# Kernel optimization log

Measured on AMD Instinct MI355X. Metric: run time of the kernel, lower is better.

Reference implementation:

```python
import math
import jax, jax.numpy as jnp
import numpy as np
from jax import lax

B, S, T = 16, 1200, 600
D, V, FF = 1024, 1404, 2048
H, DH, PERIOD, WID = 4, 256, 25, 8


def setup_inputs() -> dict:
    key = jax.random.key(0)
    ks = jax.random.split(key, 24)
    w = lambda i, shape: jax.random.normal(ks[i], shape, dtype=jnp.float32) * 0.02
    return {
        "audio_embedding": jax.random.normal(ks[0], (B, S, 768), dtype=jnp.float32),
        "vertice": jax.random.normal(ks[1], (B, T, 3, 468), dtype=jnp.float32),
        "W_af": w(2, (D, 768)), "b_af": w(3, (D,)),
        "sa_Wq": w(4, (D, D)), "sa_bq": w(5, (D,)),
        "sa_Wk": w(6, (D, D)), "sa_bk": w(7, (D,)),
        "sa_Wv": w(8, (D, D)), "sa_bv": w(9, (D,)),
        "sa_Wo": w(10, (D, D)), "sa_bo": w(11, (D,)),
        "ca_Wq": w(12, (D, D)), "ca_bq": w(13, (D,)),
        "ca_Wk": w(14, (D, D)), "ca_bk": w(15, (D,)),
        "ca_Wv": w(16, (D, D)), "ca_bv": w(17, (D,)),
        "ca_Wo": w(18, (D, D)), "ca_bo": w(19, (D,)),
        "ln1_g": jnp.ones((D,), jnp.float32), "ln1_b": jnp.zeros((D,), jnp.float32),
        "ln2_g": jnp.ones((D,), jnp.float32), "ln2_b": jnp.zeros((D,), jnp.float32),
        "ln3_g": jnp.ones((D,), jnp.float32), "ln3_b": jnp.zeros((D,), jnp.float32),
        "W_ff1": w(20, (FF, D)), "b_ff1": jnp.zeros((FF,), jnp.float32),
        "W_ff2": w(21, (D, FF)), "b_ff2": jnp.zeros((D,), jnp.float32),
        "W_vm": w(22, (D, V)), "b_vm": jnp.zeros((D,), jnp.float32),
        "W_vr": w(23, (V, D)), "b_vr": jnp.zeros((V,), jnp.float32),
    }


def _pe_table():
    # PeriodicPositionalEncoding: sin/cos table of length `period`, tiled over time
    pos = np.arange(PERIOD, dtype=np.float32)[:, None]
    div = np.exp(np.arange(0, D, 2, dtype=np.float32) * (-math.log(10000.0) / D))
    pe = np.zeros((PERIOD, D), dtype=np.float32)
    pe[:, 0::2] = np.sin(pos * div)
    pe[:, 1::2] = np.cos(pos * div)
    return jnp.asarray(pe)


def _slopes():
    start = 2.0 ** (-2.0 ** (-(math.log2(H) - 3.0)))
    return jnp.asarray(start * start ** np.arange(H, dtype=np.float32), dtype=jnp.float32)


def _ln(x, g, b):
    m = jnp.mean(x, -1, keepdims=True)
    v = jnp.mean((x - m) ** 2, -1, keepdims=True)
    return (x - m) / jnp.sqrt(v + 1e-5) * g + b


def reference(audio_embedding, vertice, W_af, b_af, sa_Wq, sa_bq, sa_Wk, sa_bk, sa_Wv, sa_bv, sa_Wo, sa_bo, ca_Wq, ca_bq, ca_Wk, ca_bk, ca_Wv, ca_bv, ca_Wo, ca_bo, ln1_g, ln1_b, ln2_g, ln2_b, ln3_g, ln3_b, W_ff1, b_ff1, W_ff2, b_ff2, W_vm, b_vm, W_vr, b_vr):
    # The torch loop reruns the full causal decoder on the growing prefix each frame;
    # because the tgt mask is strictly causal (ALiBi bias depends only on i-j), the
    # math is exactly equivalent to an incremental decode with a self-attn KV cache.
    pe, slopes = _pe_table(), _slopes()
    scale = 1.0 / math.sqrt(DH)
    NEG = -1e9
    hidden = audio_embedding @ W_af.T + b_af              # (B,S,D) audio_feature_map
    mem_k = (hidden @ ca_Wk.T + ca_bk).reshape(B, S, H, DH)
    mem_v = (hidden @ ca_Wv.T + ca_bv).reshape(B, S, H, DH)
    t_idx = jnp.arange(T)
    s_idx = jnp.arange(S)
    emb0 = jnp.broadcast_to(b_vm, (B, D))                 # vertice_map(zeros)
    kc0 = jnp.zeros((T, B, D), jnp.float32)
    vc0 = jnp.zeros((T, B, D), jnp.float32)

    def step(carry, i):
        emb, kc, vc = carry
        x = emb + pe[i % PERIOD]                          # PPE (B,D)
        q = (x @ sa_Wq.T + sa_bq).reshape(B, H, DH)
        kc = kc.at[i].set(x @ sa_Wk.T + sa_bk)
        vc = vc.at[i].set(x @ sa_Wv.T + sa_bv)
        kh = kc.reshape(T, B, H, DH)
        vh = vc.reshape(T, B, H, DH)
        rel = i - t_idx                                   # ALiBi: alibi[i,j] = -floor((i-j)/period)
        bias = slopes[:, None] * (-(jnp.maximum(rel, 0) // PERIOD)).astype(jnp.float32)
        sc = jnp.einsum('bhd,tbhd->bht', q, kh) * scale + bias[None]
        sc = jnp.where((t_idx <= i)[None, None, :], sc, NEG)
        sa = jnp.einsum('bht,tbhd->bhd', jax.nn.softmax(sc, -1), vh).reshape(B, D)
        x = _ln(x + sa @ sa_Wo.T + sa_bo, ln1_g, ln1_b)
        q2 = (x @ ca_Wq.T + ca_bq).reshape(B, H, DH)
        sc2 = jnp.einsum('bhd,bshd->bhs', q2, mem_k) * scale
        allowed = (s_idx >= 2 * i - (WID - 2)) & (s_idx < 2 * i + 2)   # enc_dec_mask window
        sc2 = jnp.where(allowed[None, None, :], sc2, NEG)
        ca = jnp.einsum('bhs,bshd->bhd', jax.nn.softmax(sc2, -1), mem_v).reshape(B, D)
        x = _ln(x + ca @ ca_Wo.T + ca_bo, ln2_g, ln2_b)
        ff = jax.nn.relu(x @ W_ff1.T + b_ff1) @ W_ff2.T + b_ff2
        x = _ln(x + ff, ln3_g, ln3_b)
        out_v = x @ W_vr.T + b_vr                         # vertice_map_r (B,V)
        emb_next = out_v @ W_vm.T + b_vm                  # vertice_map of last output
        return (emb_next, kc, vc), out_v

    _, outs = lax.scan(step, (emb0, kc0, vc0), t_idx)
    vertice_out = jnp.transpose(outs, (1, 0, 2))          # (B,T,V)
    loss = jnp.mean((vertice_out - vertice.reshape(B, T, -1)) ** 2)
    return loss
```

## Files before the change

### kernel.cpp

```cpp
#include <hip/hip_runtime.h>

typedef unsigned short u16;
typedef short s16x8 __attribute__((ext_vector_type(8)));
typedef float f32x4 __attribute__((ext_vector_type(4)));
typedef float f32x2 __attribute__((ext_vector_type(2)));

#define DEV static __device__ __forceinline__

DEV float bf2f(u16 h){ union{unsigned u;float f;} v; v.u=((unsigned)h)<<16; return v.f; }
DEV u16 f2bf(float f){ union{float f;unsigned u;} v; v.f=f; unsigned u=v.u; return (u16)((u + 0x7fffu + ((u>>16)&1u))>>16); }

DEV void st2_dc(u16* p, u16 v){
  unsigned vv = v;
  asm volatile("global_store_short %0, %1, off sc0 sc1" :: "v"(p), "v"(vv) : "memory");
}
DEV void st16_dc(void* p, s16x8 v){
  asm volatile("global_store_dwordx4 %0, %1, off sc0 sc1" :: "v"(p), "v"(v) : "memory");
}
DEV void stf_dc(float* p, float v){
  asm volatile("global_store_dword %0, %1, off sc0 sc1" :: "v"(p), "v"(v) : "memory");
}
DEV u16 ld2_dc(const u16* p){
  unsigned r;
  asm volatile("global_load_ushort %0, %1, off sc0 sc1\n\ts_waitcnt vmcnt(0)" : "=&v"(r) : "v"(p) : "memory");
  return (u16)r;
}
DEV void vmwait0(){ asm volatile("s_waitcnt vmcnt(0)" ::: "memory"); }

DEV void ldf8_dc(const u16* p, s16x8* o){
  asm volatile(
    "global_load_dwordx4 %0, %8, off sc0 sc1\n\t"
    "global_load_dwordx4 %1, %8, off offset:64 sc0 sc1\n\t"
    "global_load_dwordx4 %2, %8, off offset:128 sc0 sc1\n\t"
    "global_load_dwordx4 %3, %8, off offset:192 sc0 sc1\n\t"
    "global_load_dwordx4 %4, %8, off offset:256 sc0 sc1\n\t"
    "global_load_dwordx4 %5, %8, off offset:320 sc0 sc1\n\t"
    "global_load_dwordx4 %6, %8, off offset:384 sc0 sc1\n\t"
    "global_load_dwordx4 %7, %8, off offset:448 sc0 sc1\n\t"
    "s_waitcnt vmcnt(0)"
    : "=&v"(o[0]),"=&v"(o[1]),"=&v"(o[2]),"=&v"(o[3]),
      "=&v"(o[4]),"=&v"(o[5]),"=&v"(o[6]),"=&v"(o[7])
    : "v"(p) : "memory");
}
DEV void ldf8r_dc(const u16* p, s16x8* o, const u16* pr, unsigned* rr){
  asm volatile(
    "global_load_dwordx4 %0, %9, off sc0 sc1\n\t"
    "global_load_dwordx4 %1, %9, off offset:64 sc0 sc1\n\t"
    "global_load_dwordx4 %2, %9, off offset:128 sc0 sc1\n\t"
    "global_load_dwordx4 %3, %9, off offset:192 sc0 sc1\n\t"
    "global_load_dwordx4 %4, %9, off offset:256 sc0 sc1\n\t"
    "global_load_dwordx4 %5, %9, off offset:320 sc0 sc1\n\t"
    "global_load_dwordx4 %6, %9, off offset:384 sc0 sc1\n\t"
    "global_load_dwordx4 %7, %9, off offset:448 sc0 sc1\n\t"
    "global_load_ushort %8, %10, off sc0 sc1\n\t"
    "s_waitcnt vmcnt(0)"
    : "=&v"(o[0]),"=&v"(o[1]),"=&v"(o[2]),"=&v"(o[3]),
      "=&v"(o[4]),"=&v"(o[5]),"=&v"(o[6]),"=&v"(o[7]),"=&v"(*rr)
    : "v"(p), "v"(pr) : "memory");
}
DEV void ldf8rs_dc(const u16* p, s16x8* o, const u16* pr, unsigned* rr, const float* ps, f32x2* ss){
  asm volatile(
    "global_load_dwordx4 %0, %10, off sc0 sc1\n\t"
    "global_load_dwordx4 %1, %10, off offset:64 sc0 sc1\n\t"
    "global_load_dwordx4 %2, %10, off offset:128 sc0 sc1\n\t"
    "global_load_dwordx4 %3, %10, off offset:192 sc0 sc1\n\t"
    "global_load_dwordx4 %4, %10, off offset:256 sc0 sc1\n\t"
    "global_load_dwordx4 %5, %10, off offset:320 sc0 sc1\n\t"
    "global_load_dwordx4 %6, %10, off offset:384 sc0 sc1\n\t"
    "global_load_dwordx4 %7, %10, off offset:448 sc0 sc1\n\t"
    "global_load_ushort %8, %11, off sc0 sc1\n\t"
    "global_load_dwordx2 %9, %12, off sc0 sc1\n\t"
    "s_waitcnt vmcnt(0)"
    : "=&v"(o[0]),"=&v"(o[1]),"=&v"(o[2]),"=&v"(o[3]),
      "=&v"(o[4]),"=&v"(o[5]),"=&v"(o[6]),"=&v"(o[7]),"=&v"(*rr),"=&v"(*ss)
    : "v"(p), "v"(pr), "v"(ps) : "memory");
}
DEV void ldf16rs_dc(const u16* p, s16x8* o, const u16* pr, unsigned* rr, const float* ps, f32x2* ss){
  asm volatile(
    "global_load_dwordx4 %0, %18, off sc0 sc1\n\t"
    "global_load_dwordx4 %1, %18, off offset:64 sc0 sc1\n\t"
    "global_load_dwordx4 %2, %18, off offset:128 sc0 sc1\n\t"
    "global_load_dwordx4 %3, %18, off offset:192 sc0 sc1\n\t"
    "global_load_dwordx4 %4, %18, off offset:256 sc0 sc1\n\t"
    "global_load_dwordx4 %5, %18, off offset:320 sc0 sc1\n\t"
    "global_load_dwordx4 %6, %18, off offset:384 sc0 sc1\n\t"
    "global_load_dwordx4 %7, %18, off offset:448 sc0 sc1\n\t"
    "global_load_dwordx4 %8, %18, off offset:2048 sc0 sc1\n\t"
    "global_load_dwordx4 %9, %18, off offset:2112 sc0 sc1\n\t"
    "global_load_dwordx4 %10, %18, off offset:2176 sc0 sc1\n\t"
    "global_load_dwordx4 %11, %18, off offset:2240 sc0 sc1\n\t"
    "global_load_dwordx4 %12, %18, off offset:2304 sc0 sc1\n\t"
    "global_load_dwordx4 %13, %18, off offset:2368 sc0 sc1\n\t"
    "global_load_dwordx4 %14, %18, off offset:2432 sc0 sc1\n\t"
    "global_load_dwordx4 %15, %18, off offset:2496 sc0 sc1\n\t"
    "global_load_ushort %16, %19, off sc0 sc1\n\t"
    "global_load_dwordx2 %17, %20, off sc0 sc1\n\t"
    "s_waitcnt vmcnt(0)"
    : "=&v"(o[0]),"=&v"(o[1]),"=&v"(o[2]),"=&v"(o[3]),
      "=&v"(o[4]),"=&v"(o[5]),"=&v"(o[6]),"=&v"(o[7]),
      "=&v"(o[8]),"=&v"(o[9]),"=&v"(o[10]),"=&v"(o[11]),
      "=&v"(o[12]),"=&v"(o[13]),"=&v"(o[14]),"=&v"(o[15]),
      "=&v"(*rr),"=&v"(*ss)
    : "v"(p), "v"(pr), "v"(ps) : "memory");
}

constexpr size_t SZ_DD = (size_t)1024*1024*2;
constexpr size_t OFF_WQ=0;
constexpr size_t OFF_WK=OFF_WQ+SZ_DD;
constexpr size_t OFF_WV=OFF_WK+SZ_DD;
constexpr size_t OFF_WO=OFF_WV+SZ_DD;
constexpr size_t OFF_CAWQ=OFF_WO+SZ_DD;
constexpr size_t OFF_CAWO=OFF_CAWQ+SZ_DD;
constexpr size_t OFF_FF1=OFF_CAWO+SZ_DD;
constexpr size_t OFF_FF2=OFF_FF1+(size_t)2048*1024*2;
constexpr size_t OFF_MB =OFF_FF2+(size_t)2048*1024*2;
constexpr size_t OFF_WVR=OFF_MB+SZ_DD;
constexpr size_t OFF_WKP=OFF_WVR+(size_t)1404*1024*2;
constexpr size_t OFF_WVP=OFF_WKP+(size_t)1024*768*2;
constexpr size_t OFF_WAFT=OFF_WVP+(size_t)1024*768*2;
constexpr size_t OFF_WVRT=OFF_WAFT+(size_t)768*1024*2;
constexpr size_t OFF_PE  =OFF_WVRT+(size_t)1024*1408*2;
constexpr size_t OFF_BKP =OFF_PE+25*1024*4;
constexpr size_t OFF_BVP =OFF_BKP+4096;
constexpr size_t OFF_BCOMB=OFF_BVP+4096;
constexpr size_t OFF_MEMK=OFF_BCOMB+4096;
constexpr size_t OFF_MEMV=OFF_MEMK+(size_t)16*1200*1024*2;
constexpr size_t OFF_KC  =OFF_MEMV+(size_t)16*1200*1024*2;
constexpr size_t OFF_VC  =OFF_KC+(size_t)600*16*1024*2;
constexpr size_t OFF_U3S =OFF_VC+(size_t)600*16*1024*2;
constexpr size_t OFF_ST3 =OFF_U3S+(size_t)600*16*1024*2;
constexpr size_t OFF_EMB =OFF_ST3+600*32*4;
constexpr size_t OFF_QB  =OFF_EMB+32768;
constexpr size_t OFF_SC  =OFF_QB+32768;
constexpr size_t OFF_SA  =OFF_SC+(size_t)16*4*608*4;
constexpr size_t OFF_U1  =OFF_SA+32768;
constexpr size_t OFF_ST1 =OFF_U1+32768;
constexpr size_t OFF_Q2  =OFF_ST1+256;
constexpr size_t OFF_CA  =OFF_Q2+32768;
constexpr size_t OFF_U2  =OFF_CA+32768;
constexpr size_t OFF_ST2 =OFF_U2+32768;
constexpr size_t OFF_HH  =OFF_ST2+256;
constexpr size_t OFF_LOSS=OFF_HH+65536;
constexpr size_t OFF_BAR =OFF_LOSS+256;
constexpr size_t WS_NEED =OFF_BAR+32768;

DEV float gemm_frag(const s16x8* a, const u16* slot, float* FB){
  int tid=threadIdx.x, wv=tid>>6, ln=tid&63;
  int r=ln&15, kq=ln>>4;
  int k0=wv*256 + kq*8;
  int sw=(r&7)<<3;
  const u16* bp = slot + r*1024;
  f32x4 acc={0.f,0.f,0.f,0.f};
  #pragma unroll
  for(int j=0;j<8;j++)
    acc = __builtin_amdgcn_mfma_f32_16x16x32_bf16(a[j], *(const s16x8*)(bp + ((k0+32*j)^sw)), acc, 0,0,0);
  #pragma unroll
  for(int j=0;j<4;j++) FB[wv*256 + (kq*4+j)*16 + r] = acc[j];
  __syncthreads();
  int row=tid>>4, col=tid&15;
  float s=(FB[row*16+col]+FB[256+row*16+col])+(FB[512+row*16+col]+FB[768+row*16+col]);
  __syncthreads();
  return s;
}

DEV void ln_frags(s16x8* a, const float* g, const float* be, int k0, int r, float* RB, float* STm, float* STr){
  int tid=threadIdx.x;
  float sum=0.f, sq=0.f;
  #pragma unroll
  for(int j=0;j<8;j++){
    #pragma unroll
    for(int e=0;e<8;e++){ float f=bf2f((u16)a[j][e]); sum+=f; sq+=f*f; }
  }
  RB[tid]=sum; RB[256+tid]=sq;
  __syncthreads();
  if (tid<16){
    float S=0.f,Q=0.f;
    #pragma unroll
    for(int q=0;q<16;q++){ S+=RB[tid+16*q]; Q+=RB[256+tid+16*q]; }
    float m=S*(1.f/1024.f); float var=Q*(1.f/1024.f)-m*m;
    STm[tid]=m; STr[tid]=rsqrtf(var+1e-5f);
  }
  __syncthreads();
  float m=STm[r], rs=STr[r];
  const float* gg=g+k0; const float* bb=be+k0;
  #pragma unroll
  for(int j=0;j<8;j++){
    s16x8 o;
    #pragma unroll
    for(int e=0;e<8;e++){ int k=32*j+e; float f=(bf2f((u16)a[j][e])-m)*rs*gg[k]+bb[k]; o[e]=(short)f2bf(f); }
    a[j]=o;
  }
}

DEV void copy_slot(const u16* src, int rstride, u16* dst){
  int row=threadIdx.x>>4, k0=(threadIdx.x&15)<<6;
  int sw=(row&7)<<3;
  const u16* s = src + (size_t)row*rstride + k0;
  u16* d = dst + row*1024;
  #pragma unroll
  for(int c=0;c<64;c+=8)
    *(s16x8*)(d + (((k0+c))^sw)) = *(const s16x8*)(s+c);
}

DEV void gbar(char* barb, unsigned& epoch, int wg){
  vmwait0();
  __syncthreads();
  unsigned target = epoch + 1u;
  if (threadIdx.x == 0)
    __hip_atomic_store((unsigned*)(barb + (wg<<7)), target, __ATOMIC_RELAXED, __HIP_MEMORY_SCOPE_AGENT);
  {
    unsigned* s = (unsigned*)(barb + (threadIdx.x<<7));
    while (__hip_atomic_load(s, __ATOMIC_RELAXED, __HIP_MEMORY_SCOPE_AGENT) < target)
      __builtin_amdgcn_s_sleep(1);
  }
  __syncthreads();
  epoch++;
}

__global__ void __launch_bounds__(256) k_init(const float* b_vm, float* pe, u16* emb, float* loss, unsigned* bar){
  int tid=threadIdx.x;
  if (tid==0) loss[0]=0.f;
  for(int idx=tid; idx<8192; idx+=256) bar[idx]=0u;
  for(int idx=tid; idx<16384; idx+=256) emb[idx] = f2bf(b_vm[idx&1023]);
  for(int idx=tid; idx<25600; idx+=256){
    int p_=idx>>10, d_=idx&1023; int m=d_>>1;
    float div = expf(-(float)(2*m) * (9.210340372f/1024.f));
    float a = (float)p_ * div;
    pe[idx] = (d_&1)? cosf(a) : sinf(a);
  }
}

__global__ void __launch_bounds__(256) k_f2bf(const float* s, u16* d, int n){
  int idx=(blockIdx.x*256+threadIdx.x)*8;
  if (idx < n){
    #pragma unroll
    for(int j=0;j<8;j++) d[idx+j]=f2bf(s[idx+j]);
  }
}

__global__ void __launch_bounds__(256) k_tr(const float* src, int R, int C, u16* dst, int ldd){
  __shared__ float TL[32][33];
  int cb=(C+31)/32;
  int bj=blockIdx.x%cb, br=blockIdx.x/cb;
  int j0=bj*32, r0=br*32;
  int lj=threadIdx.x&31, lr=threadIdx.x>>5;
  #pragma unroll
  for(int p=0;p<4;p++){ int rr=r0+lr+p*8, jj=j0+lj;
    TL[lr+p*8][lj] = (rr<R && jj<C)? src[(size_t)rr*C+jj] : 0.f; }
  __syncthreads();
  #pragma unroll
  for(int p=0;p<4;p++){ int jj=j0+lr+p*8, rr=r0+lj;
    if (jj<C && rr<ldd) dst[(size_t)jj*ldd+rr] = f2bf(TL[lj][lr+p*8]); }
}

DEV float gemm_tile16g(const u16* SLu, int lds_stride, const u16* W, int Kext, int wstride, int colbase, float* FB){
  int tid=threadIdx.x, wv=tid>>6, ln=tid&63;
  int r=ln&15, kq=ln>>4;
  int kpw=Kext>>2, k0=wv*kpw;
  const u16* ap = SLu + r*lds_stride + k0 + kq*8;
  const u16* bp = W + (size_t)(colbase+r)*wstride + k0 + kq*8;
  f32x4 acc={0.f,0.f,0.f,0.f};
  for(int k=0;k<kpw;k+=32)
    acc = __builtin_amdgcn_mfma_f32_16x16x32_bf16(*(const s16x8*)(ap+k), *(const s16x8*)(bp+k), acc, 0,0,0);
  #pragma unroll
  for(int j=0;j<4;j++) FB[wv*256 + (kq*4+j)*16 + r] = acc[j];
  __syncthreads();
  int row=tid>>4, col=tid&15;
  float s=(FB[row*16+col]+FB[256+row*16+col])+(FB[512+row*16+col]+FB[768+row*16+col]);
  __syncthreads();
  return s;
}

__global__ void __launch_bounds__(256) k_gemm_pre(const float* A, int lda, int Kreal, int Kpad,
                                                  const u16* Bw, u16* out, int ldo, int Ntiles){
  __shared__ u16 SL[16*1416];
  __shared__ float FB[1024];
  int bx=blockIdx.x; int mt=bx/Ntiles, nt=bx%Ntiles;
  int tid=threadIdx.x;
  int cpt = Kpad>>4;
  { int row=tid>>4, c0=(tid&15)*cpt;
    const float* s=A + (size_t)(mt*16+row)*lda;
    u16* d=SL + row*(Kpad+8);
    for(int c=0;c<cpt;c++){ int k=c0+c; d[k] = (k<Kreal)? f2bf(s[k]) : (u16)0; }
    __syncthreads();
  }
  float v = gemm_tile16g(SL, Kpad+8, Bw, Kpad, Kpad, nt*16, FB);
  int row=tid>>4, col=tid&15;
  out[(size_t)(mt*16+row)*ldo + nt*16+col] = f2bf(v);
}

__global__ void __launch_bounds__(256) k_bvec(const float* caWk, const float* ca_bk, const float* b_af,
                                              const float* caWv, const float* ca_bv,
                                              const float* Wvm, const float* b_vr, const float* b_vm,
                                              float* bkp, float* bvp, float* bcomb){
  __shared__ float VB[1408];
  int seg=blockIdx.x>>2, ch=blockIdx.x&3; int o=ch*256+threadIdx.x;
  const float* vec = (seg==2)? b_vr : b_af; int K = (seg==2)?1404:1024;
  for(int k=threadIdx.x;k<K;k+=256) VB[k]=vec[k];
  __syncthreads();
  const float* Arow = (seg==0)? caWk+(size_t)o*1024 : (seg==1)? caWv+(size_t)o*1024 : Wvm+(size_t)o*1404;
  float s=0.f;
  for(int k=0;k<K;k++) s += Arow[k]*VB[k];
  if(seg==0) bkp[o]=s+ca_bk[o]; else if(seg==1) bvp[o]=s+ca_bv[o]; else bcomb[o]=s+b_vm[o];
}

__global__ void __launch_bounds__(256) k_mem(const float* audio, const u16* wkp, const u16* wvp,
                                             const float* bkp, const float* bvp, u16* mt8, u16* memv){
  __shared__ u16 SL[16*776];
  int bx=blockIdx.x; int mt=bx>>3, cbk=bx&7;
  int tid=threadIdx.x, wv=tid>>6, ln=tid&63;
  { int row=tid>>4, c0=(tid&15)*48;
    const float* s = audio + (size_t)(mt*16+row)*768 + c0;
    u16* d = SL + row*776 + c0;
    #pragma unroll
    for(int c=0;c<48;c+=8){ s16x8 o;
      #pragma unroll
      for(int j=0;j<8;j++) o[j]=(short)f2bf(s[c+j]);
      *(s16x8*)(d+c)=o; }
    __syncthreads();
  }
  int r=ln&15, kq=ln>>4;
  const u16* ap = SL + r*776 + kq*8;
  for(int rep=0;rep<2;rep++){
    int colb = cbk*128 + wv*32 + rep*16;
    for(int mat=0;mat<2;mat++){
      const u16* W = mat? wvp : wkp;
      const u16* bp = W + (size_t)(colb+r)*768 + kq*8;
      f32x4 acc={0.f,0.f,0.f,0.f};
      for(int k=0;k<768;k+=32)
        acc = __builtin_amdgcn_mfma_f32_16x16x32_bf16(*(const s16x8*)(ap+k), *(const s16x8*)(bp+k), acc, 0,0,0);
      const float* bias = mat? bvp:bkp;
      int o = colb + r;
      float bo = bias[o];
      #pragma unroll
      for(int j=0;j<4;j++){ int row_=kq*4+j;
        int g = mt*16+row_;
        float val = acc[j] + bo;
        if (mat){
          memv[(size_t)g*1024 + o] = f2bf(val);
        } else {
          int bb=g/1200, ss=g-bb*1200;
          mt8[(((size_t)(bb*4 + (o>>8))*32 + ((o&255)>>3))*1200 + ss)*8 + (o&7)] = f2bf(val);
        }
      }
    }
  }
}

struct LoopArgs {
  const float *sa_bq,*sa_bk,*sa_bv,*sa_bo,*ca_bq,*ca_bo,*b_ff1,*b_ff2;
  const float *g1,*be1,*g2,*be2,*g3,*be3;
  char* ws;
};

__global__ void __launch_bounds__(256,1) k_loop(LoopArgs A){
  __shared__ u16 WL[3*16*1024];
  __shared__ float FB[1024];
  __shared__ float PL[608];
  __shared__ float RB[640];
  __shared__ float STm[16], STr[16];

  char* ws = A.ws;
  const u16* wq   =(const u16*)(ws+OFF_WQ);
  const u16* wk   =(const u16*)(ws+OFF_WK);
  const u16* wv_  =(const u16*)(ws+OFF_WV);
  const u16* wo   =(const u16*)(ws+OFF_WO);
  const u16* cawq =(const u16*)(ws+OFF_CAWQ);
  const u16* cawo =(const u16*)(ws+OFF_CAWO);
  const u16* ff1  =(const u16*)(ws+OFF_FF1);
  const u16* ff2  =(const u16*)(ws+OFF_FF2);
  const u16* mb   =(const u16*)(ws+OFF_MB);
  const float* pe =(const float*)(ws+OFF_PE);
  const float* bcomb=(const float*)(ws+OFF_BCOMB);
  const u16* mt8  =(const u16*)(ws+OFF_MEMK);
  const u16* memv =(const u16*)(ws+OFF_MEMV);
  u16* kc =(u16*)(ws+OFF_KC);
  u16* vc =(u16*)(ws+OFF_VC);
  u16* u3s=(u16*)(ws+OFF_U3S);
  float* st3=(float*)(ws+OFF_ST3);
  u16* emb=(u16*)(ws+OFF_EMB);
  u16* qb =(u16*)(ws+OFF_QB);
  u16* sab=(u16*)(ws+OFF_SA);
  u16* u1 =(u16*)(ws+OFF_U1);
  float* st1=(float*)(ws+OFF_ST1);
  u16* q2b=(u16*)(ws+OFF_Q2);
  u16* cab=(u16*)(ws+OFF_CA);
  u16* u2 =(u16*)(ws+OFF_U2);
  float* st2=(float*)(ws+OFF_ST2);
  u16* hh =(u16*)(ws+OFF_HH);
  char* barb=(char*)(ws+OFF_BAR);

  unsigned epoch = 0;
  int wg = blockIdx.x, tid = threadIdx.x;
  int row = tid>>4, lo = tid&15;
  int wv = tid>>6, ln = tid&63;
  int fr = ln&15, kq = ln>>4;
  int k0 = wv*256 + kq*8;
  int grp = wg>>6, ct = (wg&63)<<4;

  {
    u16* s0d = WL;          u16* s1d = WL+16384;  u16* s2d = WL+32768;
    if (grp==0){
      copy_slot(wq  +(size_t)ct*1024,1024,s0d);
      copy_slot(cawq+(size_t)ct*1024,1024,s1d);
      copy_slot(ff1 +(size_t)ct*1024,1024,s2d);
    } else if (grp==1){
      copy_slot(wk  +(size_t)ct*1024,1024,s0d);
      copy_slot(cawo+(size_t)ct*1024,1024,s1d);
      copy_slot(ff1 +((size_t)(1024+ct))*1024,1024,s2d);
    } else if (grp==2){
      copy_slot(wv_ +(size_t)ct*1024,1024,s0d);
      copy_slot(ff2 +(size_t)ct*2048,2048,s1d);
      copy_slot(ff2 +(size_t)ct*2048+1024,2048,s2d);
    } else {
      copy_slot(wo  +(size_t)ct*1024,1024,s0d);
      copy_slot(mb  +(size_t)ct*1024,1024,s1d);
    }
    __syncthreads();
  }
  const u16* SLOT0 = WL;
  const u16* SLOT1 = WL+16384;
  const u16* SLOT2 = WL+32768;

  #pragma unroll 1
  for (int i=0;i<600;i++){
    int ip = i%25;

    if (wg < 192){
      s16x8 f[8];
      ldf8_dc(emb + fr*1024 + k0, f);
      const float* pp = pe + ip*1024 + k0;
      #pragma unroll
      for(int j=0;j<8;j++){ s16x8 o;
        #pragma unroll
        for(int e=0;e<8;e++) o[e]=(short)f2bf(bf2f((u16)f[j][e]) + pp[32*j+e]);
        f[j]=o; }
      const float* bias = (grp==0)? A.sa_bq : (grp==1)? A.sa_bk : A.sa_bv;
      float v = gemm_frag(f,SLOT0,FB);
      int o = ct + lo;
      u16 bv = f2bf(v + bias[o]);
      if (grp==0)      st2_dc(qb + row*1024 + o, bv);
      else if (grp==1) st2_dc(kc + ((size_t)i*16+row)*1024 + o, bv);
      else             st2_dc(vc + ((size_t)i*16+row)*1024 + o, bv);
    }
    gbar(barb, epoch, wg);

    if (wg < 64){
      int b=wg>>2, h=wg&3, cnt=i+1;
      RB[tid] = bf2f(ld2_dc(qb + b*1024 + h*256 + tid));
      __syncthreads();
      float sl = 1.0f/(float)(4<<(2*h));
      float mloc=-1e30f, lloc=0.f;
      for(int t=tid; t<cnt; t+=256){
        const u16* kr = kc + ((size_t)t*16 + b)*1024 + h*256;
        float s=0.f;
        #pragma unroll
        for(int c=0;c<256;c+=8){
          s16x8 k8 = *(const s16x8*)(kr+c);
          #pragma unroll
          for(int j=0;j<8;j++) s += RB[c+j]*bf2f((u16)k8[j]);
        }
        s = s*0.0625f - sl*(float)((i-t)/25);
        PL[t]=s;
        float M = fmaxf(mloc, s);
        lloc = lloc*__expf(mloc-M) + __expf(s-M);
        mloc = M;
      }
      #pragma unroll
      for(int off=32; off>0; off>>=1){
        float m2=__shfl_xor(mloc,off), l2=__shfl_xor(lloc,off);
        float M=fmaxf(mloc,m2);
        lloc = lloc*__expf(mloc-M) + l2*__expf(m2-M);
        mloc = M;
      }
      if (ln==0){ RB[576+2*wv]=mloc; RB[577+2*wv]=lloc; }
      __syncthreads();
      float M=-1e30f, L=0.f;
      #pragma unroll
      for(int w=0;w<4;w++){
        float m2=RB[576+2*w], l2=RB[577+2*w];
        float Mn=fmaxf(M,m2);
        L = L*__expf(M-Mn) + l2*__expf(m2-Mn);
        M = Mn;
      }
      float rl = 1.0f/L;
      int d_oct = tid>>3, t_ln = tid&7;
      const u16* vcb = vc + (size_t)b*1024 + h*256 + d_oct*8;
      float acc[8]={0.f,0.f,0.f,0.f,0.f,0.f,0.f,0.f};
      for(int t=t_ln; t<cnt; t+=8){
        s16x8 v8 = *(const s16x8*)(vcb + (size_t)t*16384);
        float p = __expf(PL[t]-M);
        #pragma unroll
        for(int jj=0;jj<8;jj++) acc[jj] += p*bf2f((u16)v8[jj]);
      }
      #pragma unroll
      for(int j=0;j<8;j++){
        acc[j] += __shfl_xor(acc[j],1);
        acc[j] += __shfl_xor(acc[j],2);
        acc[j] += __shfl_xor(acc[j],4);
      }
      if (t_ln==0){
        s16x8 o8;
        #pragma unroll
        for(int j=0;j<8;j++) o8[j]=(short)f2bf(acc[j]*rl);
        st16_dc(sab + b*1024 + h*256 + d_oct*8, o8);
      }
    }
    gbar(barb, epoch, wg);

    if (wg>=192){
      s16x8 f[8]; unsigned er;
      ldf8r_dc(sab + fr*1024 + k0, f, emb + row*1024 + ct + lo, &er);
      float v = gemm_frag(f,SLOT0,FB);
      int o = ct+lo;
      float x = bf2f((u16)er) + pe[ip*1024+o];
      st2_dc(u1 + row*1024 + o, f2bf(x + v + A.sa_bo[o]));
    }
    gbar(barb, epoch, wg);

    if (wg<64){
      s16x8 f[8];
      ldf8_dc(u1 + fr*1024 + k0, f);
      ln_frags(f, A.g1, A.be1, k0, fr, RB, STm, STr);
      float v = gemm_frag(f,SLOT1,FB);
      int o=ct+lo;
      st2_dc(q2b + row*1024+o, f2bf(v + A.ca_bq[o]));
      if (wg==0 && tid<16){ stf_dc(st1+tid*2, STm[tid]); stf_dc(st1+tid*2+1, STr[tid]); }
    }
    gbar(barb, epoch, wg);

    if (wg<64){
      int b=wg>>2, h=wg&3;
      RB[tid] = bf2f(ld2_dc(q2b + b*1024 + h*256 + tid));
      __syncthreads();
      int s0 = 2*i-6; if(s0<0)s0=0;
      int s1 = 2*i+2; if(s1>1200)s1=1200;
      int ns = s1-s0;
      int si=tid>>5, dl=tid&31;
      float p=0.f;
      if (si<ns){
        const u16* MT = mt8 + (((size_t)(b*4+h)*32 + dl)*1200 + (s0+si))*8;
        s16x8 m8 = *(const s16x8*)MT;
        #pragma unroll
        for(int j=0;j<8;j++) p += RB[dl*8+j]*bf2f((u16)m8[j]);
      }
      #pragma unroll
      for(int o2=16;o2>0;o2>>=1) p += __shfl_xor(p,o2);
      if (dl==0 && si<ns) RB[512+si] = p*0.0625f;
      __syncthreads();
      float mx=-1e30f;
      for(int q=0;q<ns;q++) mx=fmaxf(mx,RB[512+q]);
      float l=0.f, acc=0.f;
      for(int q=0;q<ns;q++){
        float e=__expf(RB[512+q]-mx); l+=e;
        acc += e*bf2f(memv[(size_t)(b*1200+s0+q)*1024 + h*256 + tid]);
      }
      st2_dc(cab + b*1024+h*256+tid, f2bf(acc/l));
    }
    gbar(barb, epoch, wg);

    if (wg>=64 && wg<128){
      s16x8 f[8]; unsigned ur; f32x2 sv;
      ldf8rs_dc(cab + fr*1024 + k0, f, u1 + row*1024 + ct + lo, &ur, st1 + row*2, &sv);
      float v = gemm_frag(f,SLOT1,FB);
      int o=ct+lo;
      float x1 = (bf2f((u16)ur)-sv[0])*sv[1]*A.g1[o] + A.be1[o];
      st2_dc(u2+row*1024+o, f2bf(x1 + v + A.ca_bo[o]));
    }
    gbar(barb, epoch, wg);

    if (wg<128){
      s16x8 f[8];
      ldf8_dc(u2 + fr*1024 + k0, f);
      ln_frags(f, A.g2, A.be2, k0, fr, RB, STm, STr);
      float v = gemm_frag(f,SLOT2,FB);
      int o=(wg<<4)+lo;
      st2_dc(hh+row*2048+o, f2bf(fmaxf(v + A.b_ff1[o], 0.f)));
      if (wg==0 && tid<16){ stf_dc(st2+tid*2,STm[tid]); stf_dc(st2+tid*2+1,STr[tid]); }
    }
    gbar(barb, epoch, wg);

    if (wg>=128 && wg<192){
      s16x8 f[16]; unsigned ur; f32x2 sv;
      ldf16rs_dc(hh + fr*2048 + k0, f, u2 + row*1024 + ct + lo, &ur, st2 + row*2, &sv);
      float v = gemm_frag(f,SLOT1,FB);
      v += gemm_frag(f+8,SLOT2,FB);
      int o=ct+lo;
      float x2 = (bf2f((u16)ur)-sv[0])*sv[1]*A.g2[o] + A.be2[o];
      st2_dc(u3s + ((size_t)i*16+row)*1024+o, f2bf(x2 + v + A.b_ff2[o]));
    }
    gbar(barb, epoch, wg);

    if (wg>=192){
      s16x8 f[8];
      ldf8_dc(u3s + (size_t)i*16384 + fr*1024 + k0, f);
      ln_frags(f, A.g3, A.be3, k0, fr, RB, STm, STr);
      float v = gemm_frag(f,SLOT1,FB);
      int o=ct+lo;
      st2_dc(emb+row*1024+o, f2bf(v + bcomb[o]));
      if (wg==192 && tid<16){ st3[i*32+tid*2]=STm[tid]; st3[i*32+tid*2+1]=STr[tid]; }
    }
    gbar(barb, epoch, wg);
  }
}

__global__ void __launch_bounds__(256) k_loss(const u16* u3s, const float* st3, const u16* wvr,
                                              const float* bvr, const float* g3, const float* be3,
                                              const float* vert, float* loss){
  __shared__ u16 SL[16*1032];
  __shared__ float R[64];
  int bx=blockIdx.x; int ib=bx/11, cb=bx%11;
  int tid=threadIdx.x, wvv=tid>>6, ln=tid&63;
  int r=ln&15, kq=ln>>4;
  float lsum=0.f;
  for(int ii=0;ii<8;ii++){
    int i=ib*8+ii;
    { int row=tid>>4, c0=(tid&15)<<6;
      float m=st3[i*32+row*2], rs=st3[i*32+row*2+1];
      const u16* s=u3s + (size_t)(i*16+row)*1024 + c0;
      u16* d=SL + row*1032 + c0;
      #pragma unroll
      for(int c=0;c<64;c+=8){ s16x8 v=*(const s16x8*)(s+c); s16x8 o;
        #pragma unroll
        for(int j=0;j<8;j++){ int cc=c0+c+j; o[j]=(short)f2bf((bf2f((u16)v[j])-m)*rs*g3[cc]+be3[cc]); }
        *(s16x8*)(d+c)=o; }
      __syncthreads();
    }
    const u16* ap = SL + r*1032 + kq*8;
    for(int rep=0;rep<2;rep++){
      int colb = cb*128 + wvv*32 + rep*16;
      int o_r = colb + r; bool ok = o_r < 1404;
      const u16* bp = wvr + (size_t)(ok? o_r:0)*1024 + kq*8;
      f32x4 acc={0.f,0.f,0.f,0.f};
      for(int k=0;k<1024;k+=32)
        acc = __builtin_amdgcn_mfma_f32_16x16x32_bf16(*(const s16x8*)(ap+k), *(const s16x8*)(bp+k), acc, 0,0,0);
      if (ok){
        float bo = bvr[o_r];
        #pragma unroll
        for(int j=0;j<4;j++){
          int b_=kq*4+j;
          float ov = acc[j] + bo;
          float vt = vert[(size_t)(b_*600 + i)*1404 + o_r];
          float dd = ov - vt; lsum += dd*dd;
        }
      }
    }
    __syncthreads();
  }
  #pragma unroll
  for(int o=32;o>0;o>>=1) lsum += __shfl_down(lsum,o);
  if (ln==0) R[wvv]=lsum;
  __syncthreads();
  if (tid==0) atomicAdd(loss, (R[0]+R[1])+(R[2]+R[3]));
}

__global__ void k_fin(const float* loss, float* dout){
  if (threadIdx.x==0) dout[0] = loss[0] * (1.f/13478400.f);
}

extern "C" void kernel_launch(void* const* d_in, const int* in_sizes, int n_in,
                              void* d_out, int out_size, void* d_ws, size_t ws_size,
                              hipStream_t stream){
  char* ws = (char*)d_ws;
  if (ws_size < WS_NEED){ hipMemsetAsync(d_out, 0, 4, stream); return; }

  const float* audio=(const float*)d_in[0];
  const float* vert =(const float*)d_in[1];
  const float* W_af =(const float*)d_in[2];
  const float* b_af =(const float*)d_in[3];
  const float* saWq =(const float*)d_in[4];  const float* sa_bq=(const float*)d_in[5];
  const float* saWk =(const float*)d_in[6];  const float* sa_bk=(const float*)d_in[7];
  const float* saWv =(const float*)d_in[8];  const float* sa_bv=(const float*)d_in[9];
  const float* saWo =(const float*)d_in[10]; const float* sa_bo=(const float*)d_in[11];
  const float* caWq =(const float*)d_in[12]; const float* ca_bq=(const float*)d_in[13];
  const float* caWk =(const float*)d_in[14]; const float* ca_bk=(const float*)d_in[15];
  const float* caWv =(const float*)d_in[16]; const float* ca_bv=(const float*)d_in[17];
  const float* caWo =(const float*)d_in[18]; const float* ca_bo=(const float*)d_in[19];
  const float* g1=(const float*)d_in[20]; const float* be1=(const float*)d_in[21];
  const float* g2=(const float*)d_in[22]; const float* be2=(const float*)d_in[23];
  const float* g3=(const float*)d_in[24]; const float* be3=(const float*)d_in[25];
  const float* Wff1=(const float*)d_in[26]; const float* b_ff1=(const float*)d_in[27];
  const float* Wff2=(const float*)d_in[28]; const float* b_ff2=(const float*)d_in[29];
  const float* Wvm=(const float*)d_in[30];  const float* b_vm=(const float*)d_in[31];
  const float* Wvr=(const float*)d_in[32];  const float* b_vr=(const float*)d_in[33];

  k_init<<<1,256,0,stream>>>(b_vm, (float*)(ws+OFF_PE), (u16*)(ws+OFF_EMB), (float*)(ws+OFF_LOSS), (unsigned*)(ws+OFF_BAR));

  k_f2bf<<<512,256,0,stream>>>(saWq,(u16*)(ws+OFF_WQ),1048576);
  k_f2bf<<<512,256,0,stream>>>(saWk,(u16*)(ws+OFF_WK),1048576);
  k_f2bf<<<512,256,0,stream>>>(saWv,(u16*)(ws+OFF_WV),1048576);
  k_f2bf<<<512,256,0,stream>>>(saWo,(u16*)(ws+OFF_WO),1048576);
  k_f2bf<<<512,256,0,stream>>>(caWq,(u16*)(ws+OFF_CAWQ),1048576);
  k_f2bf<<<512,256,0,stream>>>(caWo,(u16*)(ws+OFF_CAWO),1048576);
  k_f2bf<<<1024,256,0,stream>>>(Wff1,(u16*)(ws+OFF_FF1),2097152);
  k_f2bf<<<1024,256,0,stream>>>(Wff2,(u16*)(ws+OFF_FF2),2097152);
  k_f2bf<<<702,256,0,stream>>>(Wvr,(u16*)(ws+OFF_WVR),1437696);

  k_tr<<<24*32,256,0,stream>>>(W_af, 1024, 768, (u16*)(ws+OFF_WAFT), 1024);
  k_tr<<<32*44,256,0,stream>>>(Wvr, 1404, 1024, (u16*)(ws+OFF_WVRT), 1408);

  k_gemm_pre<<<64*48,256,0,stream>>>(caWk, 1024, 1024, 1024, (const u16*)(ws+OFF_WAFT), (u16*)(ws+OFF_WKP), 768, 48);
  k_gemm_pre<<<64*48,256,0,stream>>>(caWv, 1024, 1024, 1024, (const u16*)(ws+OFF_WAFT), (u16*)(ws+OFF_WVP), 768, 48);
  k_gemm_pre<<<64*64,256,0,stream>>>(Wvm, 1404, 1404, 1408, (const u16*)(ws+OFF_WVRT), (u16*)(ws+OFF_MB), 1024, 64);

  k_bvec<<<12,256,0,stream>>>(caWk, ca_bk, b_af, caWv, ca_bv, Wvm, b_vr, b_vm,
                              (float*)(ws+OFF_BKP),(float*)(ws+OFF_BVP),(float*)(ws+OFF_BCOMB));

  k_mem<<<9600,256,0,stream>>>(audio, (const u16*)(ws+OFF_WKP),(const u16*)(ws+OFF_WVP),
                               (const float*)(ws+OFF_BKP),(const float*)(ws+OFF_BVP),
                               (u16*)(ws+OFF_MEMK),(u16*)(ws+OFF_MEMV));

  LoopArgs la{ sa_bq, sa_bk, sa_bv, sa_bo, ca_bq, ca_bo, b_ff1, b_ff2,
               g1, be1, g2, be2, g3, be3, ws };
  k_loop<<<256,256,0,stream>>>(la);

  k_loss<<<825,256,0,stream>>>((const u16*)(ws+OFF_U3S),(const float*)(ws+OFF_ST3),
                               (const u16*)(ws+OFF_WVR), b_vr, g3, be3, vert, (float*)(ws+OFF_LOSS));
  k_fin<<<1,64,0,stream>>>((const float*)(ws+OFF_LOSS), (float*)d_out);
}
```

Baseline: 36.21 ms.

## Fold vertice-map into self-attn QKV weights and fuse cross-attn Q into attention phase

Precomputes fused weights (Wq·Mb, Wk·Mb, Wv·Mb) and per-period positional bias tables so that the next step's Q/K/V are produced directly from the final LayerNorm output in the last phase of each step, removing a whole grid-barrier phase. The cross-attention query projection with LN1 is also computed inside the attention workgroups (scalar dot product over bf16 weights) instead of in its own barrier phase. Fewer global barriers per step should reduce latency in the persistent loop. In exchange there is extra setup work, bf16 rounding of the folded weight products, and a scalar matvec in the attention workgroups.

```diff
diff --git a/kernel.cpp b/kernel.cpp
--- a/kernel.cpp
+++ b/kernel.cpp
@@ -4,6 +4,7 @@
 typedef short s16x8 __attribute__((ext_vector_type(8)));
 typedef float f32x4 __attribute__((ext_vector_type(4)));
 typedef float f32x2 __attribute__((ext_vector_type(2)));
+typedef unsigned u32x2 __attribute__((ext_vector_type(2)));
 
 #define DEV static __device__ __forceinline__
 
@@ -24,6 +25,11 @@
   unsigned r;
   asm volatile("global_load_ushort %0, %1, off sc0 sc1\n\ts_waitcnt vmcnt(0)" : "=&v"(r) : "v"(p) : "memory");
   return (u16)r;
+}
+DEV u32x2 ld8_dc2(const u16* p){
+  u32x2 r;
+  asm volatile("global_load_dwordx2 %0, %1, off sc0 sc1\n\ts_waitcnt vmcnt(0)" : "=&v"(r) : "v"(p) : "memory");
+  return r;
 }
 DEV void vmwait0(){ asm volatile("s_waitcnt vmcnt(0)" ::: "memory"); }
 
@@ -105,10 +111,10 @@
 }
 
 constexpr size_t SZ_DD = (size_t)1024*1024*2;
-constexpr size_t OFF_WQ=0;
-constexpr size_t OFF_WK=OFF_WQ+SZ_DD;
-constexpr size_t OFF_WV=OFF_WK+SZ_DD;
-constexpr size_t OFF_WO=OFF_WV+SZ_DD;
+constexpr size_t OFF_WQ2=0;
+constexpr size_t OFF_WK2=OFF_WQ2+SZ_DD;
+constexpr size_t OFF_WV2=OFF_WK2+SZ_DD;
+constexpr size_t OFF_WO=OFF_WV2+SZ_DD;
 constexpr size_t OFF_CAWQ=OFF_WO+SZ_DD;
 constexpr size_t OFF_CAWO=OFF_CAWQ+SZ_DD;
 constexpr size_t OFF_FF1=OFF_CAWO+SZ_DD;
@@ -129,8 +135,8 @@
 constexpr size_t OFF_VC  =OFF_KC+(size_t)600*16*1024*2;
 constexpr size_t OFF_U3S =OFF_VC+(size_t)600*16*1024*2;
 constexpr size_t OFF_ST3 =OFF_U3S+(size_t)600*16*1024*2;
-constexpr size_t OFF_EMB =OFF_ST3+600*32*4;
-constexpr size_t OFF_QB  =OFF_EMB+32768;
+constexpr size_t OFF_XB  =OFF_ST3+600*32*4;
+constexpr size_t OFF_QB  =OFF_XB+32768;
 constexpr size_t OFF_SC  =OFF_QB+32768;
 constexpr size_t OFF_SA  =OFF_SC+(size_t)16*4*608*4;
 constexpr size_t OFF_U1  =OFF_SA+32768;
@@ -142,7 +148,9 @@
 constexpr size_t OFF_HH  =OFF_ST2+256;
 constexpr size_t OFF_LOSS=OFF_HH+65536;
 constexpr size_t OFF_BAR =OFF_LOSS+256;
-constexpr size_t WS_NEED =OFF_BAR+32768;
+constexpr size_t OFF_MBT =OFF_BAR+32768;
+constexpr size_t OFF_AT  =OFF_MBT+SZ_DD;
+constexpr size_t WS_NEED =OFF_AT+(size_t)3*25*1024*4;
 
 DEV float gemm_frag(const s16x8* a, const u16* slot, float* FB){
   int tid=threadIdx.x, wv=tid>>6, ln=tid&63;
@@ -217,11 +225,10 @@
   epoch++;
 }
 
-__global__ void __launch_bounds__(256) k_init(const float* b_vm, float* pe, u16* emb, float* loss, unsigned* bar){
+__global__ void __launch_bounds__(256) k_init(float* pe, float* loss, unsigned* bar){
   int tid=threadIdx.x;
   if (tid==0) loss[0]=0.f;
   for(int idx=tid; idx<8192; idx+=256) bar[idx]=0u;
-  for(int idx=tid; idx<16384; idx+=256) emb[idx] = f2bf(b_vm[idx&1023]);
   for(int idx=tid; idx<25600; idx+=256){
     int p_=idx>>10, d_=idx&1023; int m=d_>>1;
     float div = expf(-(float)(2*m) * (9.210340372f/1024.f));
@@ -251,6 +258,17 @@
   #pragma unroll
   for(int p=0;p<4;p++){ int jj=j0+lr+p*8, rr=r0+lj;
     if (jj<C && rr<ldd) dst[(size_t)jj*ldd+rr] = f2bf(TL[lj][lr+p*8]); }
+}
+
+__global__ void __launch_bounds__(256) k_trb(const u16* src, u16* dst){
+  __shared__ u16 T[32][33];
+  int bi=blockIdx.x>>5, bj=blockIdx.x&31;
+  int li=threadIdx.x>>5, lj=threadIdx.x&31;
+  #pragma unroll
+  for(int p=0;p<4;p++) T[li+p*8][lj] = src[(size_t)(bi*32+li+p*8)*1024 + bj*32+lj];
+  __syncthreads();
+  #pragma unroll
+  for(int p=0;p<4;p++) dst[(size_t)(bj*32+li+p*8)*1024 + bi*32+lj] = T[lj][li+p*8];
 }
 
 DEV float gemm_tile16g(const u16* SLu, int lds_stride, const u16* W, int Kext, int wstride, int colbase, float* FB){
@@ -302,6 +320,47 @@
   float s=0.f;
   for(int k=0;k<K;k++) s += Arow[k]*VB[k];
   if(seg==0) bkp[o]=s+ca_bk[o]; else if(seg==1) bvp[o]=s+ca_bv[o]; else bcomb[o]=s+b_vm[o];
+}
+
+__global__ void __launch_bounds__(256) k_afold(const float* pe, const float* bcomb,
+                                               const float* Wq, const float* Wk, const float* Wv,
+                                               const float* bq, const float* bk, const float* bv,
+                                               float* at){
+  __shared__ float XV[1024];
+  int bx=blockIdx.x; int mat=bx/100; int rem=bx%100; int ip=rem>>2; int ch=rem&3;
+  const float* W = (mat==0)?Wq:(mat==1)?Wk:Wv;
+  const float* bias = (mat==0)?bq:(mat==1)?bk:bv;
+  for(int o=threadIdx.x;o<1024;o+=256) XV[o]=bcomb[o]+pe[ip*1024+o];
+  __syncthreads();
+  int c = ch*256+threadIdx.x;
+  const float* wr = W + (size_t)c*1024;
+  float acc=0.f;
+  for(int o=0;o<1024;o++) acc += XV[o]*wr[o];
+  at[((size_t)mat*25+ip)*1024+c] = acc + bias[c];
+}
+
+__global__ void __launch_bounds__(256) k_qkv0(const float* b_vm, const float* pe,
+                                              const float* Wq, const float* Wk, const float* Wv,
+                                              const float* bq, const float* bk, const float* bv,
+                                              u16* qb, u16* kc, u16* vc, u16* xb){
+  __shared__ float XV[1024];
+  int bx=blockIdx.x; int mat=bx&3, ch=bx>>2;
+  for(int o=threadIdx.x;o<1024;o+=256) XV[o]=b_vm[o]+pe[o];
+  __syncthreads();
+  int c = ch*256+threadIdx.x;
+  if (mat==3){
+    u16 hv = f2bf(XV[c]);
+    for(int r=0;r<16;r++) xb[r*1024+c]=hv;
+  } else {
+    const float* W = (mat==0)?Wq:(mat==1)?Wk:Wv;
+    const float* bias = (mat==0)?bq:(mat==1)?bk:bv;
+    const float* wr = W + (size_t)c*1024;
+    float acc=0.f;
+    for(int o=0;o<1024;o++) acc += XV[o]*wr[o];
+    u16 hv = f2bf(acc + bias[c]);
+    u16* dst = (mat==0)? qb : (mat==1)? kc : vc;
+    for(int r=0;r<16;r++) dst[r*1024+c]=hv;
+  }
 }
 
 __global__ void __launch_bounds__(256) k_mem(const float* audio, const u16* wkp, const u16* wvp,
@@ -348,7 +407,7 @@
 }
 
 struct LoopArgs {
-  const float *sa_bq,*sa_bk,*sa_bv,*sa_bo,*ca_bq,*ca_bo,*b_ff1,*b_ff2;
+  const float *sa_bo,*ca_bq,*ca_bo,*b_ff1,*b_ff2;
   const float *g1,*be1,*g2,*be2,*g3,*be3;
   char* ws;
 };
@@ -361,9 +420,9 @@
   __shared__ float STm[16], STr[16];
 
   char* ws = A.ws;
-  const u16* wq   =(const u16*)(ws+OFF_WQ);
-  const u16* wk   =(const u16*)(ws+OFF_WK);
-  const u16* wv_  =(const u16*)(ws+OFF_WV);
+  const u16* wq2  =(const u16*)(ws+OFF_WQ2);
+  const u16* wk2  =(const u16*)(ws+OFF_WK2);
+  const u16* wv2  =(const u16*)(ws+OFF_WV2);
   const u16* wo   =(const u16*)(ws+OFF_WO);
   const u16* cawq =(const u16*)(ws+OFF_CAWQ);
   const u16* cawo =(const u16*)(ws+OFF_CAWO);
@@ -372,18 +431,18 @@
   const u16* mb   =(const u16*)(ws+OFF_MB);
   const float* pe =(const float*)(ws+OFF_PE);
   const float* bcomb=(const float*)(ws+OFF_BCOMB);
+  const float* at =(const float*)(ws+OFF_AT);
   const u16* mt8  =(const u16*)(ws+OFF_MEMK);
   const u16* memv =(const u16*)(ws+OFF_MEMV);
   u16* kc =(u16*)(ws+OFF_KC);
   u16* vc =(u16*)(ws+OFF_VC);
   u16* u3s=(u16*)(ws+OFF_U3S);
   float* st3=(float*)(ws+OFF_ST3);
-  u16* emb=(u16*)(ws+OFF_EMB);
+  u16* xb =(u16*)(ws+OFF_XB);
   u16* qb =(u16*)(ws+OFF_QB);
   u16* sab=(u16*)(ws+OFF_SA);
   u16* u1 =(u16*)(ws+OFF_U1);
   float* st1=(float*)(ws+OFF_ST1);
-  u16* q2b=(u16*)(ws+OFF_Q2);
   u16* cab=(u16*)(ws+OFF_CA);
   u16* u2 =(u16*)(ws+OFF_U2);
   float* st2=(float*)(ws+OFF_ST2);
@@ -401,20 +460,19 @@
   {
     u16* s0d = WL;          u16* s1d = WL+16384;  u16* s2d = WL+32768;
     if (grp==0){
-      copy_slot(wq  +(size_t)ct*1024,1024,s0d);
-      copy_slot(cawq+(size_t)ct*1024,1024,s1d);
+      copy_slot(wq2 +(size_t)ct*1024,1024,s0d);
       copy_slot(ff1 +(size_t)ct*1024,1024,s2d);
     } else if (grp==1){
-      copy_slot(wk  +(size_t)ct*1024,1024,s0d);
+      copy_slot(wk2 +(size_t)ct*1024,1024,s0d);
       copy_slot(cawo+(size_t)ct*1024,1024,s1d);
       copy_slot(ff1 +((size_t)(1024+ct))*1024,1024,s2d);
     } else if (grp==2){
-      copy_slot(wv_ +(size_t)ct*1024,1024,s0d);
+      copy_slot(wv2 +(size_t)ct*1024,1024,s0d);
       copy_slot(ff2 +(size_t)ct*2048,2048,s1d);
       copy_slot(ff2 +(size_t)ct*2048+1024,2048,s2d);
     } else {
-      copy_slot(wo  +(size_t)ct*1024,1024,s0d);
-      copy_slot(mb  +(size_t)ct*1024,1024,s1d);
+      copy_slot(mb  +(size_t)ct*1024,1024,s0d);
+      copy_slot(wo  +(size_t)ct*1024,1024,s1d);
     }
     __syncthreads();
   }
@@ -424,26 +482,6 @@
 
   #pragma unroll 1
   for (int i=0;i<600;i++){
-    int ip = i%25;
-
-    if (wg < 192){
-      s16x8 f[8];
-      ldf8_dc(emb + fr*1024 + k0, f);
-      const float* pp = pe + ip*1024 + k0;
-      #pragma unroll
-      for(int j=0;j<8;j++){ s16x8 o;
-        #pragma unroll
-        for(int e=0;e<8;e++) o[e]=(short)f2bf(bf2f((u16)f[j][e]) + pp[32*j+e]);
-        f[j]=o; }
-      const float* bias = (grp==0)? A.sa_bq : (grp==1)? A.sa_bk : A.sa_bv;
-      float v = gemm_frag(f,SLOT0,FB);
-      int o = ct + lo;
-      u16 bv = f2bf(v + bias[o]);
-      if (grp==0)      st2_dc(qb + row*1024 + o, bv);
-      else if (grp==1) st2_dc(kc + ((size_t)i*16+row)*1024 + o, bv);
-      else             st2_dc(vc + ((size_t)i*16+row)*1024 + o, bv);
-    }
-    gbar(barb, epoch, wg);
 
     if (wg < 64){
       int b=wg>>2, h=wg&3, cnt=i+1;
@@ -510,28 +548,45 @@
 
     if (wg>=192){
       s16x8 f[8]; unsigned er;
-      ldf8r_dc(sab + fr*1024 + k0, f, emb + row*1024 + ct + lo, &er);
-      float v = gemm_frag(f,SLOT0,FB);
+      ldf8r_dc(sab + fr*1024 + k0, f, xb + row*1024 + ct + lo, &er);
+      float v = gemm_frag(f,SLOT1,FB);
       int o = ct+lo;
-      float x = bf2f((u16)er) + pe[ip*1024+o];
-      st2_dc(u1 + row*1024 + o, f2bf(x + v + A.sa_bo[o]));
-    }
-    gbar(barb, epoch, wg);
-
-    if (wg<64){
-      s16x8 f[8];
-      ldf8_dc(u1 + fr*1024 + k0, f);
-      ln_frags(f, A.g1, A.be1, k0, fr, RB, STm, STr);
-      float v = gemm_frag(f,SLOT1,FB);
-      int o=ct+lo;
-      st2_dc(q2b + row*1024+o, f2bf(v + A.ca_bq[o]));
-      if (wg==0 && tid<16){ stf_dc(st1+tid*2, STm[tid]); stf_dc(st1+tid*2+1, STr[tid]); }
+      st2_dc(u1 + row*1024 + o, f2bf(bf2f((u16)er) + v + A.sa_bo[o]));
     }
     gbar(barb, epoch, wg);
 
     if (wg<64){
       int b=wg>>2, h=wg&3;
-      RB[tid] = bf2f(ld2_dc(q2b + b*1024 + h*256 + tid));
+      u32x2 uu = ld8_dc2(u1 + b*1024 + tid*4);
+      float e0=bf2f((u16)(uu[0]&0xffffu)), e1=bf2f((u16)(uu[0]>>16));
+      float e2=bf2f((u16)(uu[1]&0xffffu)), e3=bf2f((u16)(uu[1]>>16));
+      float s=(e0+e1)+(e2+e3);
+      float q=(e0*e0+e1*e1)+(e2*e2+e3*e3);
+      #pragma unroll
+      for(int o2=32;o2>0;o2>>=1){ s+=__shfl_down(s,o2); q+=__shfl_down(q,o2); }
+      if (ln==0){ RB[608+wv]=s; RB[616+wv]=q; }
+      __syncthreads();
+      float S=(RB[608]+RB[609])+(RB[610]+RB[611]);
+      float Q=(RB[616]+RB[617])+(RB[618]+RB[619]);
+      float m=S*(1.f/1024.f);
+      float rs=rsqrtf(Q*(1.f/1024.f)-m*m+1e-5f);
+      if (h==0 && tid==0){ stf_dc(st1+b*2, m); stf_dc(st1+b*2+1, rs); }
+      { int k=tid*4;
+        FB[k]  =(e0-m)*rs*A.g1[k]  +A.be1[k];
+        FB[k+1]=(e1-m)*rs*A.g1[k+1]+A.be1[k+1];
+        FB[k+2]=(e2-m)*rs*A.g1[k+2]+A.be1[k+2];
+        FB[k+3]=(e3-m)*rs*A.g1[k+3]+A.be1[k+3]; }
+      __syncthreads();
+      int c = h*256 + tid;
+      const u16* wr = cawq + (size_t)c*1024;
+      float acc=0.f;
+      #pragma unroll 4
+      for(int kk=0;kk<128;kk++){
+        s16x8 w8 = *(const s16x8*)(wr + kk*8);
+        #pragma unroll
+        for(int j=0;j<8;j++) acc += FB[kk*8+j]*bf2f((u16)w8[j]);
+      }
+      RB[tid] = acc + A.ca_bq[c];
       __syncthreads();
       int s0 = 2*i-6; if(s0<0)s0=0;
       int s1 = 2*i+2; if(s1>1200)s1=1200;
@@ -549,13 +604,13 @@
       if (dl==0 && si<ns) RB[512+si] = p*0.0625f;
       __syncthreads();
       float mx=-1e30f;
-      for(int q=0;q<ns;q++) mx=fmaxf(mx,RB[512+q]);
-      float l=0.f, acc=0.f;
-      for(int q=0;q<ns;q++){
-        float e=__expf(RB[512+q]-mx); l+=e;
-        acc += e*bf2f(memv[(size_t)(b*1200+s0+q)*1024 + h*256 + tid]);
-      }
-      st2_dc(cab + b*1024+h*256+tid, f2bf(acc/l));
+      for(int qd=0;qd<ns;qd++) mx=fmaxf(mx,RB[512+qd]);
+      float l=0.f, acc2=0.f;
+      for(int qd=0;qd<ns;qd++){
+        float e=__expf(RB[512+qd]-mx); l+=e;
+        acc2 += e*bf2f(memv[(size_t)(b*1200+s0+qd)*1024 + h*256 + tid]);
+      }
+      st2_dc(cab + b*1024+h*256+tid, f2bf(acc2/l));
     }
     gbar(barb, epoch, wg);
 
@@ -591,14 +646,23 @@
     }
     gbar(barb, epoch, wg);
 
-    if (wg>=192){
+    {
+      int ipn = (i+1)%25;
       s16x8 f[8];
       ldf8_dc(u3s + (size_t)i*16384 + fr*1024 + k0, f);
       ln_frags(f, A.g3, A.be3, k0, fr, RB, STm, STr);
-      float v = gemm_frag(f,SLOT1,FB);
-      int o=ct+lo;
-      st2_dc(emb+row*1024+o, f2bf(v + bcomb[o]));
-      if (wg==192 && tid<16){ st3[i*32+tid*2]=STm[tid]; st3[i*32+tid*2+1]=STr[tid]; }
+      float v = gemm_frag(f,SLOT0,FB);
+      int o = ct+lo;
+      if (grp==0){
+        st2_dc(qb + row*1024 + o, f2bf(v + at[(size_t)0*25600 + ipn*1024 + o]));
+      } else if (grp==1){
+        if (i<599) st2_dc(kc + ((size_t)(i+1)*16+row)*1024 + o, f2bf(v + at[(size_t)1*25600 + ipn*1024 + o]));
+      } else if (grp==2){
+        if (i<599) st2_dc(vc + ((size_t)(i+1)*16+row)*1024 + o, f2bf(v + at[(size_t)2*25600 + ipn*1024 + o]));
+      } else {
+        st2_dc(xb + row*1024 + o, f2bf(v + bcomb[o] + pe[ipn*1024+o]));
+        if (wg==192 && tid<16){ st3[i*32+tid*2]=STm[tid]; st3[i*32+tid*2+1]=STr[tid]; }
+      }
     }
     gbar(barb, epoch, wg);
   }
@@ -684,14 +748,11 @@
   const float* Wvm=(const float*)d_in[30];  const float* b_vm=(const float*)d_in[31];
   const float* Wvr=(const float*)d_in[32];  const float* b_vr=(const float*)d_in[33];
 
-  k_init<<<1,256,0,stream>>>(b_vm, (float*)(ws+OFF_PE), (u16*)(ws+OFF_EMB), (float*)(ws+OFF_LOSS), (unsigned*)(ws+OFF_BAR));
-
-  k_f2bf<<<512,256,0,stream>>>(saWq,(u16*)(ws+OFF_WQ),1048576);
-  k_f2bf<<<512,256,0,stream>>>(saWk,(u16*)(ws+OFF_WK),1048576);
-  k_f2bf<<<512,256,0,stream>>>(saWv,(u16*)(ws+OFF_WV),1048576);
-  k_f2bf<<<512,256,0,stream>>>(saWo,(u16*)(ws+OFF_WO),1048576);
+  k_init<<<1,256,0,stream>>>((float*)(ws+OFF_PE), (float*)(ws+OFF_LOSS), (unsigned*)(ws+OFF_BAR));
+
   k_f2bf<<<512,256,0,stream>>>(caWq,(u16*)(ws+OFF_CAWQ),1048576);
   k_f2bf<<<512,256,0,stream>>>(caWo,(u16*)(ws+OFF_CAWO),1048576);
+  k_f2bf<<<512,256,0,stream>>>(saWo,(u16*)(ws+OFF_WO),1048576);
   k_f2bf<<<1024,256,0,stream>>>(Wff1,(u16*)(ws+OFF_FF1),2097152);
   k_f2bf<<<1024,256,0,stream>>>(Wff2,(u16*)(ws+OFF_FF2),2097152);
   k_f2bf<<<702,256,0,stream>>>(Wvr,(u16*)(ws+OFF_WVR),1437696);
@@ -703,14 +764,25 @@
   k_gemm_pre<<<64*48,256,0,stream>>>(caWv, 1024, 1024, 1024, (const u16*)(ws+OFF_WAFT), (u16*)(ws+OFF_WVP), 768, 48);
   k_gemm_pre<<<64*64,256,0,stream>>>(Wvm, 1404, 1404, 1408, (const u16*)(ws+OFF_WVRT), (u16*)(ws+OFF_MB), 1024, 64);
 
+  k_trb<<<1024,256,0,stream>>>((const u16*)(ws+OFF_MB), (u16*)(ws+OFF_MBT));
+  k_gemm_pre<<<64*64,256,0,stream>>>(saWq, 1024, 1024, 1024, (const u16*)(ws+OFF_MBT), (u16*)(ws+OFF_WQ2), 1024, 64);
+  k_gemm_pre<<<64*64,256,0,stream>>>(saWk, 1024, 1024, 1024, (const u16*)(ws+OFF_MBT), (u16*)(ws+OFF_WK2), 1024, 64);
+  k_gemm_pre<<<64*64,256,0,stream>>>(saWv, 1024, 1024, 1024, (const u16*)(ws+OFF_MBT), (u16*)(ws+OFF_WV2), 1024, 64);
+
   k_bvec<<<12,256,0,stream>>>(caWk, ca_bk, b_af, caWv, ca_bv, Wvm, b_vr, b_vm,
                               (float*)(ws+OFF_BKP),(float*)(ws+OFF_BVP),(float*)(ws+OFF_BCOMB));
+
+  k_afold<<<300,256,0,stream>>>((const float*)(ws+OFF_PE), (const float*)(ws+OFF_BCOMB),
+                                saWq, saWk, saWv, sa_bq, sa_bk, sa_bv, (float*)(ws+OFF_AT));
+
+  k_qkv0<<<16,256,0,stream>>>(b_vm, (const float*)(ws+OFF_PE), saWq, saWk, saWv, sa_bq, sa_bk, sa_bv,
+                              (u16*)(ws+OFF_QB), (u16*)(ws+OFF_KC), (u16*)(ws+OFF_VC), (u16*)(ws+OFF_XB));
 
   k_mem<<<9600,256,0,stream>>>(audio, (const u16*)(ws+OFF_WKP),(const u16*)(ws+OFF_WVP),
                                (const float*)(ws+OFF_BKP),(const float*)(ws+OFF_BVP),
                                (u16*)(ws+OFF_MEMK),(u16*)(ws+OFF_MEMV));
 
-  LoopArgs la{ sa_bq, sa_bk, sa_bv, sa_bo, ca_bq, ca_bo, b_ff1, b_ff2,
+  LoopArgs la{ sa_bo, ca_bq, ca_bo, b_ff1, b_ff2,
                g1, be1, g2, be2, g3, be3, ws };
   k_loop<<<256,256,0,stream>>>(la);
 
```

Result: slower. 41.64 ms (+15.0%).
